# Kernel optimization log

Hardware: AMD Instinct MI355X
Metric: run time of the kernel (lower is better)

Reference implementation:

```python
import jax, jax.numpy as jnp
import numpy as np

B, S, D = 16, 2048, 512

def setup_inputs() -> dict:
    key = jax.random.key(0)
    ks = jax.random.split(key, 8)
    # xavier_uniform bound for [1,S,S]: sqrt(6/(S+S))
    bnd_attn = float(np.sqrt(6.0 / (S + S)))
    bnd_lin = float(np.sqrt(6.0 / (D + D)))
    return {
        "query": jax.random.normal(ks[0], (B, S, D), dtype=jnp.float32),
        "key": jax.random.normal(ks[1], (B, S, D), dtype=jnp.float32),
        "value": jax.random.normal(ks[2], (B, S, D), dtype=jnp.float32),
        "attn_bias": jax.random.uniform(ks[3], (1, S, S), minval=-bnd_attn, maxval=bnd_attn, dtype=jnp.float32),
        "Wq": jax.random.uniform(ks[4], (D, D), minval=-bnd_lin, maxval=bnd_lin, dtype=jnp.float32),
        "bq": jnp.zeros((D,), dtype=jnp.float32),
        "Wk": jax.random.uniform(ks[5], (D, D), minval=-bnd_lin, maxval=bnd_lin, dtype=jnp.float32),
        "bk": jnp.zeros((D,), dtype=jnp.float32),
    }

def reference(query, key, value, attn_bias, Wq, bq, Wk, bk):
    # q = query_fc(query); k = key_fc(key)  (torch Linear: x @ W.T + b)
    q = jnp.einsum('bsd,ed->bse', query, Wq) + bq            # [B,S,D]
    k = jnp.einsum('bsd,ed->bse', key, Wk) + bk              # [B,S,D]
    scores = attn_bias + jnp.einsum('bqd,bkd->bqk', q, k)    # [B,S,S]
    attention = jax.nn.softmax(scores, axis=-1)              # [B,S,S]
    out = jnp.einsum('bqk,bkd->bqd', attention, value)       # [B,S,D] (raw value, per source)
    return (out, attention)
```

## Files before the change

kernel.cpp:

```cpp
#include <hip/hip_runtime.h>


#define Bsz 16
#define Ssz 2048
#define Dsz 512
#define BK 32

#define AS1 __attribute__((address_space(1)))
#define AS3 __attribute__((address_space(3)))

typedef short bhalf8 __attribute__((ext_vector_type(8)));
typedef float f32x4 __attribute__((ext_vector_type(4)));
typedef unsigned short u16;

__device__ __forceinline__ u16 bf16_rn(float x) {
  unsigned u = __builtin_bit_cast(unsigned, x);
  u += 0x7fffu + ((u >> 16) & 1u);
  return (u16)(u >> 16);
}
__device__ __forceinline__ float bf16_f(u16 h) {
  unsigned u = ((unsigned)h) << 16;
  return __builtin_bit_cast(float, u);
}
__device__ __forceinline__ void gload16(const void* g, void* l) {
  __builtin_amdgcn_global_load_lds((const AS1 void*)g, (AS3 void*)l, 16, 0, 0);
}
__device__ __forceinline__ unsigned pk_bf16(float x, float y) {
  return (unsigned)bf16_rn(x) | ((unsigned)bf16_rn(y) << 16);
}

__global__ __launch_bounds__(256) void prep_w(const float* __restrict__ Wq,
                                              const float* __restrict__ Wk,
                                              u16* __restrict__ WTh,
                                              u16* __restrict__ WTl) {
  const int n = blockIdx.x >> 1;
  const int k = ((blockIdx.x & 1) << 8) + threadIdx.x;
  float acc = 0.f;
  for (int e = 0; e < Dsz; ++e)
    acc = fmaf(Wq[e * Dsz + k], Wk[e * Dsz + n], acc);
  const u16 h = bf16_rn(acc);
  WTh[n * Dsz + k] = h;
  WTl[n * Dsz + k] = bf16_rn(acc - bf16_f(h));
}

__global__ __launch_bounds__(256) void split_pair(const float* __restrict__ x,
                                                  u16* __restrict__ xh,
                                                  u16* __restrict__ xl, int n4) {
  const int i = blockIdx.x * 256 + threadIdx.x;
  if (i >= n4) return;
  const float4 v = ((const float4*)x)[i];
  const float xs[4] = {v.x, v.y, v.z, v.w};
  ushort4 h, l;
  u16* hp = (u16*)&h; u16* lp = (u16*)&l;
#pragma unroll
  for (int q = 0; q < 4; ++q) {
    hp[q] = bf16_rn(xs[q]);
    lp[q] = bf16_rn(xs[q] - bf16_f(hp[q]));
  }
  ((ushort4*)xh)[i] = h;
  ((ushort4*)xl)[i] = l;
}

__global__ __launch_bounds__(256) void transpose_v(const float* __restrict__ v,
                                                   u16* __restrict__ vT) {
  __shared__ u16 tile[64][65];
  const int b = blockIdx.z;
  const int d0 = blockIdx.x * 64, k0 = blockIdx.y * 64;
  const int c = threadIdx.x & 63, r4 = threadIdx.x >> 6;
  const float* vb = v + (long long)b * Ssz * Dsz;
  u16* vTb = vT + (long long)b * Dsz * Ssz;
#pragma unroll
  for (int p = 0; p < 16; ++p) {
    const int r = p * 4 + r4;
    tile[r][c] = bf16_rn(vb[(long long)(k0 + r) * Dsz + d0 + c]);
  }
  __syncthreads();
#pragma unroll
  for (int p = 0; p < 16; ++p) {
    const int cc = p * 4 + r4;
    vTb[(long long)(d0 + cc) * Ssz + k0 + c] = tile[c][cc];
  }
}

__global__ __launch_bounds__(256) void zero_f(float* __restrict__ p, int n) {
  const int i = blockIdx.x * 256 + threadIdx.x;
  if (i < n) p[i] = 0.f;
}

template <bool SPLIT_OUT>
__global__ __launch_bounds__(256) void gemm_split(
    const u16* __restrict__ Ahg, const u16* __restrict__ Alg, int lda, long long sA,
    const u16* __restrict__ Bhg, const u16* __restrict__ Blg, int ldb, long long sB,
    float* __restrict__ C, u16* __restrict__ Ch, u16* __restrict__ Cl, int ldc,
    long long sC, const float* __restrict__ bias, int K) {
  __shared__ u16 Ah[128 * 32], Al[128 * 32], Bh[128 * 32], Bl[128 * 32];
  const int tid = threadIdx.x, ln = tid & 63, wv = tid >> 6;
  const int wm = wv >> 1, wn = wv & 1;
  const int col = ln & 15, quad = ln >> 4;
  const int m0 = blockIdx.y * 128, n0 = blockIdx.x * 128;
  const long long z = blockIdx.z;
  const u16* Ahb = Ahg + z * sA; const u16* Alb = Alg + z * sA;
  const u16* Bhb = Bhg + z * sB; const u16* Blb = Blg + z * sB;

  long long aoff[2], boff[2];
  int lbase[2];
#pragma unroll
  for (int p = 0; p < 2; ++p) {
    const int cid = p * 256 + tid;
    const int row = cid >> 2;
    const int cg = (cid & 3) ^ ((row >> 1) & 3);
    aoff[p] = (long long)(m0 + row) * lda + cg * 8;
    boff[p] = (long long)(n0 + row) * ldb + cg * 8;
    lbase[p] = (p * 256 + wv * 64) * 8;
  }
  const int fsw = quad ^ ((col >> 1) & 3);
  const int aro = (wm * 64 + col) * 32 + fsw * 8;
  const int bro = (wn * 64 + col) * 32 + fsw * 8;

  f32x4 acc[4][4] = {};

  for (int kc = 0; kc < K; kc += BK) {
    __syncthreads();
#pragma unroll
    for (int p = 0; p < 2; ++p) {
      gload16(Ahb + aoff[p] + kc, &Ah[lbase[p]]);
      gload16(Alb + aoff[p] + kc, &Al[lbase[p]]);
      gload16(Bhb + boff[p] + kc, &Bh[lbase[p]]);
      gload16(Blb + boff[p] + kc, &Bl[lbase[p]]);
    }
    __syncthreads();
    bhalf8 ah[4], al[4], bh[4], bl[4];
#pragma unroll
    for (int i = 0; i < 4; ++i) {
      ah[i] = *(const bhalf8*)&Ah[aro + i * 16 * 32];
      al[i] = *(const bhalf8*)&Al[aro + i * 16 * 32];
      bh[i] = *(const bhalf8*)&Bh[bro + i * 16 * 32];
      bl[i] = *(const bhalf8*)&Bl[bro + i * 16 * 32];
    }
#pragma unroll
    for (int i = 0; i < 4; ++i)
#pragma unroll
      for (int j = 0; j < 4; ++j) {
        acc[i][j] = __builtin_amdgcn_mfma_f32_16x16x32_bf16(ah[i], bh[j], acc[i][j], 0, 0, 0);
        acc[i][j] = __builtin_amdgcn_mfma_f32_16x16x32_bf16(ah[i], bl[j], acc[i][j], 0, 0, 0);
        acc[i][j] = __builtin_amdgcn_mfma_f32_16x16x32_bf16(al[i], bh[j], acc[i][j], 0, 0, 0);
      }
  }

#pragma unroll
  for (int i = 0; i < 4; ++i) {
    const int mb = m0 + wm * 64 + (i << 4) + (quad << 2);
#pragma unroll
    for (int j = 0; j < 4; ++j) {
      const int n = n0 + wn * 64 + (j << 4) + col;
#pragma unroll
      for (int r = 0; r < 4; ++r) {
        const int m = mb + r;
        const float v = acc[i][j][r];
        if (SPLIT_OUT) {
          const u16 h = bf16_rn(v);
          Ch[(long long)m * ldc + n] = h;
          Cl[(long long)m * ldc + n] = bf16_rn(v - bf16_f(h));
        } else {
          C[z * sC + (long long)m * ldc + n] =
              v + bias[(long long)m * Ssz + n];
        }
      }
    }
  }
}

__global__ __launch_bounds__(256) void gemm_scores(
    const u16* __restrict__ Ahg, const u16* __restrict__ Alg,
    const u16* __restrict__ Bhg, const u16* __restrict__ Blg,
    const float* __restrict__ bias, float* __restrict__ C,
    float* __restrict__ rowsum) {
  __shared__ u16 Ah[128 * 32], Al[128 * 32], Bh[128 * 32], Bl[128 * 32];
  const int tid = threadIdx.x, ln = tid & 63, wv = tid >> 6;
  const int wm = wv >> 1, wn = wv & 1;
  const int col = ln & 15, quad = ln >> 4;
  const int m0 = blockIdx.y * 128, n0 = blockIdx.x * 128;
  const long long z = blockIdx.z;
  const long long zo = z * (long long)Ssz * Dsz;
  const u16* Ahb = Ahg + zo; const u16* Alb = Alg + zo;
  const u16* Bhb = Bhg + zo; const u16* Blb = Blg + zo;

  long long aoff[2], boff[2];
  int lbase[2];
#pragma unroll
  for (int p = 0; p < 2; ++p) {
    const int cid = p * 256 + tid;
    const int row = cid >> 2;
    const int cg = (cid & 3) ^ ((row >> 1) & 3);
    aoff[p] = (long long)(m0 + row) * Dsz + cg * 8;
    boff[p] = (long long)(n0 + row) * Dsz + cg * 8;
    lbase[p] = (p * 256 + wv * 64) * 8;
  }
  const int fsw = quad ^ ((col >> 1) & 3);
  const int aro = (wm * 64 + col) * 32 + fsw * 8;
  const int bro = (wn * 64 + col) * 32 + fsw * 8;

  f32x4 acc[4][4] = {};

  for (int kc = 0; kc < Dsz; kc += BK) {
    __syncthreads();
#pragma unroll
    for (int p = 0; p < 2; ++p) {
      gload16(Ahb + aoff[p] + kc, &Ah[lbase[p]]);
      gload16(Alb + aoff[p] + kc, &Al[lbase[p]]);
      gload16(Bhb + boff[p] + kc, &Bh[lbase[p]]);
      gload16(Blb + boff[p] + kc, &Bl[lbase[p]]);
    }
    __syncthreads();
    bhalf8 ah[4], al[4], bh[4], bl[4];
#pragma unroll
    for (int i = 0; i < 4; ++i) {
      ah[i] = *(const bhalf8*)&Ah[aro + i * 16 * 32];
      al[i] = *(const bhalf8*)&Al[aro + i * 16 * 32];
      bh[i] = *(const bhalf8*)&Bh[bro + i * 16 * 32];
      bl[i] = *(const bhalf8*)&Bl[bro + i * 16 * 32];
    }
#pragma unroll
    for (int i = 0; i < 4; ++i)
#pragma unroll
      for (int j = 0; j < 4; ++j) {
        acc[i][j] = __builtin_amdgcn_mfma_f32_16x16x32_bf16(ah[i], bh[j], acc[i][j], 0, 0, 0);
        acc[i][j] = __builtin_amdgcn_mfma_f32_16x16x32_bf16(ah[i], bl[j], acc[i][j], 0, 0, 0);
        acc[i][j] = __builtin_amdgcn_mfma_f32_16x16x32_bf16(al[i], bh[j], acc[i][j], 0, 0, 0);
      }
  }

  float* Cb = C + z * (long long)Ssz * Ssz;
  float* rsb = rowsum + z * Ssz;
#pragma unroll
  for (int i = 0; i < 4; ++i) {
    const int mb = m0 + wm * 64 + (i << 4) + (quad << 2);
#pragma unroll
    for (int r = 0; r < 4; ++r) {
      const int m = mb + r;
      float rs = 0.f;
#pragma unroll
      for (int j = 0; j < 4; ++j) {
        const int n = n0 + wn * 64 + (j << 4) + col;
        const float s = acc[i][j][r] + bias[(long long)m * Ssz + n];
        const float e = __expf(fminf(s - 80.f, 80.f));
        Cb[(long long)m * Ssz + n] = e;
        rs += e;
      }
      rs += __shfl_xor(rs, 1);
      rs += __shfl_xor(rs, 2);
      rs += __shfl_xor(rs, 4);
      rs += __shfl_xor(rs, 8);
      if (col == 0) atomicAdd(&rsb[m], rs);
    }
  }
}

__global__ __launch_bounds__(1024, 4) void pv_fused(
    float* __restrict__ attn,
    const float* __restrict__ rowsum,
    const u16* __restrict__ vT,
    float* __restrict__ out) {
  __shared__ u16 Vlds[2 * 16384];
  __shared__ u16 Plds[128 * 40];

  const int tid = threadIdx.x, ln = tid & 63, wv = tid >> 6;
  const int col = ln & 15, quad = ln >> 4;
  const int bid = blockIdx.x;
  const int xcd = bid & 7, k8 = bid >> 3;
  const int z = 2 * xcd + (k8 >> 4);
  const int m0 = (k8 & 15) * 128;

  float* Sb = attn + (long long)z * Ssz * Ssz + (long long)m0 * Ssz;
  const u16* vTb = vT + (long long)z * Dsz * Ssz;

  const int er = tid >> 3, es = tid & 7;
  const float eil = 1.0f / rowsum[(long long)z * Ssz + m0 + er];
  float* Srow = Sb + (long long)er * Ssz;

  int voff[2], vlb[2];
#pragma unroll
  for (int p = 0; p < 2; ++p) {
    const int q = p * 1024 + tid;
    const int row = q >> 2;
    const int cg = (q & 3) ^ ((row >> 1) & 3);
    voff[p] = row * Ssz + cg * 8;
    vlb[p] = (p * 1024 + wv * 64) * 8;
  }
  const int wm = wv >> 2, wn = wv & 3;
  const int apo = (wm * 32 + col) * 40;
  const int fsw = quad ^ ((col >> 1) & 3);
  const int bro = (wn * 128 + col) * 32 + fsw * 8;

  f32x4 acc[2][8] = {};

#pragma unroll
  for (int p = 0; p < 2; ++p) gload16(vTb + voff[p], &Vlds[vlb[p]]);
  float4 curS = *(const float4*)(Srow + es * 4);

  for (int t = 0; t < 64; ++t) {
    const int kc = t * 32, vb = t & 1;
    __syncthreads();
    float4 nextS = curS;
    if (t < 63) {
#pragma unroll
      for (int p = 0; p < 2; ++p)
        gload16(vTb + voff[p] + kc + 32, &Vlds[(vb ^ 1) * 16384 + vlb[p]]);
      nextS = *(const float4*)(Srow + kc + 32 + es * 4);
    }
    float4 p4;
    p4.x = curS.x * eil;
    p4.y = curS.y * eil;
    p4.z = curS.z * eil;
    p4.w = curS.w * eil;
    *(float4*)(Srow + kc + es * 4) = p4;
    uint2 pk;
    pk.x = pk_bf16(p4.x, p4.y);
    pk.y = pk_bf16(p4.z, p4.w);
    *(uint2*)&Plds[er * 40 + es * 4] = pk;
    asm volatile("s_waitcnt lgkmcnt(0)" ::: "memory");
    __builtin_amdgcn_s_barrier();
    asm volatile("" ::: "memory");
    bhalf8 pa[2];
#pragma unroll
    for (int i = 0; i < 2; ++i)
      pa[i] = *(const bhalf8*)&Plds[apo + i * 16 * 40 + quad * 8];
    __builtin_amdgcn_s_setprio(1);
#pragma unroll
    for (int j = 0; j < 8; ++j) {
      const bhalf8 vbv = *(const bhalf8*)&Vlds[vb * 16384 + bro + j * 16 * 32];
      acc[0][j] = __builtin_amdgcn_mfma_f32_16x16x32_bf16(pa[0], vbv, acc[0][j], 0, 0, 0);
      acc[1][j] = __builtin_amdgcn_mfma_f32_16x16x32_bf16(pa[1], vbv, acc[1][j], 0, 0, 0);
    }
    __builtin_amdgcn_s_setprio(0);
    curS = nextS;
  }

  float* ob = out + (long long)z * Ssz * Dsz;
#pragma unroll
  for (int i = 0; i < 2; ++i) {
    const int mb = m0 + wm * 32 + (i << 4) + (quad << 2);
#pragma unroll
    for (int j = 0; j < 8; ++j) {
      const int d = wn * 128 + (j << 4) + col;
#pragma unroll
      for (int r = 0; r < 4; ++r)
        ob[(long long)(mb + r) * Dsz + d] = acc[i][j][r];
    }
  }
}

extern "C" void kernel_launch(void* const* d_in, const int* in_sizes, int n_in,
                              void* d_out, int out_size, void* d_ws, size_t ws_size,
                              hipStream_t stream) {
  const float* query = (const float*)d_in[0];
  const float* key   = (const float*)d_in[1];
  const float* value = (const float*)d_in[2];
  const float* bias  = (const float*)d_in[3];
  const float* Wq    = (const float*)d_in[4];
  const float* Wk    = (const float*)d_in[6];

  float* outR  = (float*)d_out;
  float* attnR = outR + (long long)Bsz * Ssz * Dsz;

  u16* th = (u16*)outR;
  u16* tl = th + (long long)Bsz * Ssz * Dsz;

  char* w = (char*)d_ws;
  u16* vT  = (u16*)w;                                   w += (size_t)Bsz * Dsz * Ssz * 2;
  u16* WTh = (u16*)w;                                   w += (size_t)Dsz * Dsz * 2;
  u16* WTl = (u16*)w;                                   w += (size_t)Dsz * Dsz * 2;
  u16* qkh = (u16*)w;                                   w += (size_t)Bsz * Ssz * Dsz * 2;
  u16* qkl = (u16*)w;

  float* rowsum = (float*)WTh;

  const int nQK = Bsz * Ssz * Dsz;

  prep_w<<<dim3(1024), 256, 0, stream>>>(Wq, Wk, WTh, WTl);
  transpose_v<<<dim3(Dsz / 64, Ssz / 64, Bsz), 256, 0, stream>>>(value, vT);
  split_pair<<<dim3(nQK / 4 / 256), 256, 0, stream>>>(query, qkh, qkl, nQK / 4);

  gemm_split<true><<<dim3(Dsz / 128, (Bsz * Ssz) / 128, 1), 256, 0, stream>>>(
      qkh, qkl, Dsz, 0, WTh, WTl, Dsz, 0,
      nullptr, th, tl, Dsz, 0, nullptr, Dsz);

  split_pair<<<dim3(nQK / 4 / 256), 256, 0, stream>>>(key, qkh, qkl, nQK / 4);

  zero_f<<<dim3((Bsz * Ssz + 255) / 256), 256, 0, stream>>>(rowsum, Bsz * Ssz);

  gemm_scores<<<dim3(Ssz / 128, Ssz / 128, Bsz), 256, 0, stream>>>(
      th, tl, qkh, qkl, bias, attnR, rowsum);

  pv_fused<<<dim3(256), dim3(1024), 0, stream>>>(attnR, rowsum, vT, outR);
}
```

Before: 1.048 ms.

## Store unnormalized scores as bf16 workspace and write normalized attention in PV

```diff
diff --git a/kernel.cpp b/kernel.cpp
--- a/kernel.cpp
+++ b/kernel.cpp
@@ -170,6 +170,198 @@
   }
 }
 
+__global__ __launch_bounds__(256) void gemm_scores_b16(
+    const u16* __restrict__ Ahg, const u16* __restrict__ Alg,
+    const u16* __restrict__ Bhg, const u16* __restrict__ Blg,
+    const float* __restrict__ bias, u16* __restrict__ e16,
+    float* __restrict__ rowsum) {
+  __shared__ u16 Ah[128 * 32], Al[128 * 32], Bh[128 * 32], Bl[128 * 32];
+  const int tid = threadIdx.x, ln = tid & 63, wv = tid >> 6;
+  const int wm = wv >> 1, wn = wv & 1;
+  const int col = ln & 15, quad = ln >> 4;
+  const int bid = blockIdx.x;
+  const int sb = bid >> 8, wi = bid & 255;
+  const long long z = wi & 15;
+  const int n0 = ((sb & 3) * 4 + ((wi >> 4) & 3)) * 128;
+  const int m0 = ((sb >> 2) * 4 + (wi >> 6)) * 128;
+
+  const long long zo = z * (long long)Ssz * Dsz;
+  const u16* Ahb = Ahg + zo; const u16* Alb = Alg + zo;
+  const u16* Bhb = Bhg + zo; const u16* Blb = Blg + zo;
+
+  long long aoff[2], boff[2];
+  int lbase[2];
+#pragma unroll
+  for (int p = 0; p < 2; ++p) {
+    const int cid = p * 256 + tid;
+    const int row = cid >> 2;
+    const int cg = (cid & 3) ^ ((row >> 1) & 3);
+    aoff[p] = (long long)(m0 + row) * Dsz + cg * 8;
+    boff[p] = (long long)(n0 + row) * Dsz + cg * 8;
+    lbase[p] = (p * 256 + wv * 64) * 8;
+  }
+  const int fsw = quad ^ ((col >> 1) & 3);
+  const int aro = (wm * 64 + col) * 32 + fsw * 8;
+  const int bro = (wn * 64 + col) * 32 + fsw * 8;
+
+  f32x4 acc[4][4] = {};
+
+  for (int kc = 0; kc < Dsz; kc += BK) {
+    __syncthreads();
+#pragma unroll
+    for (int p = 0; p < 2; ++p) {
+      gload16(Ahb + aoff[p] + kc, &Ah[lbase[p]]);
+      gload16(Alb + aoff[p] + kc, &Al[lbase[p]]);
+      gload16(Bhb + boff[p] + kc, &Bh[lbase[p]]);
+      gload16(Blb + boff[p] + kc, &Bl[lbase[p]]);
+    }
+    __syncthreads();
+    bhalf8 ah[4], al[4], bh[4], bl[4];
+#pragma unroll
+    for (int i = 0; i < 4; ++i) {
+      ah[i] = *(const bhalf8*)&Ah[aro + i * 16 * 32];
+      al[i] = *(const bhalf8*)&Al[aro + i * 16 * 32];
+      bh[i] = *(const bhalf8*)&Bh[bro + i * 16 * 32];
+      bl[i] = *(const bhalf8*)&Bl[bro + i * 16 * 32];
+    }
+#pragma unroll
+    for (int i = 0; i < 4; ++i)
+#pragma unroll
+      for (int j = 0; j < 4; ++j) {
+        acc[i][j] = __builtin_amdgcn_mfma_f32_16x16x32_bf16(ah[i], bh[j], acc[i][j], 0, 0, 0);
+        acc[i][j] = __builtin_amdgcn_mfma_f32_16x16x32_bf16(ah[i], bl[j], acc[i][j], 0, 0, 0);
+        acc[i][j] = __builtin_amdgcn_mfma_f32_16x16x32_bf16(al[i], bh[j], acc[i][j], 0, 0, 0);
+      }
+  }
+
+  u16* Eb = e16 + z * (long long)Ssz * Ssz;
+  float* rsb = rowsum + z * Ssz;
+#pragma unroll
+  for (int i = 0; i < 4; ++i) {
+    const int mb = m0 + wm * 64 + (i << 4) + (quad << 2);
+#pragma unroll
+    for (int r = 0; r < 4; ++r) {
+      const int m = mb + r;
+      float rs = 0.f;
+#pragma unroll
+      for (int j = 0; j < 4; ++j) {
+        const int n = n0 + wn * 64 + (j << 4) + col;
+        const float s = acc[i][j][r] + bias[(long long)m * Ssz + n];
+        const u16 h = bf16_rn(__expf(fminf(s - 80.f, 80.f)));
+        Eb[(long long)m * Ssz + n] = h;
+        rs += bf16_f(h);
+      }
+      rs += __shfl_xor(rs, 1);
+      rs += __shfl_xor(rs, 2);
+      rs += __shfl_xor(rs, 4);
+      rs += __shfl_xor(rs, 8);
+      if (col == 0) atomicAdd(&rsb[m], rs);
+    }
+  }
+}
+
+__global__ __launch_bounds__(1024, 4) void pv_fused_b16(
+    const u16* __restrict__ e16,
+    const float* __restrict__ rowsum,
+    const u16* __restrict__ vT,
+    float* __restrict__ attn,
+    float* __restrict__ out) {
+  __shared__ u16 Elds[2 * 4096];
+  __shared__ u16 Vlds[2 * 16384];
+
+  const int tid = threadIdx.x, ln = tid & 63, wv = tid >> 6;
+  const int col = ln & 15, quad = ln >> 4;
+  const int bid = blockIdx.x;
+  const int xcd = bid & 7, k8 = bid >> 3;
+  const int z = 2 * xcd + (k8 >> 4);
+  const int m0 = (k8 & 15) * 128;
+
+  const u16* Eb = e16 + (long long)z * Ssz * Ssz + (long long)m0 * Ssz;
+  const u16* vTb = vT + (long long)z * Dsz * Ssz;
+  float* Pb = attn + (long long)z * Ssz * Ssz + (long long)m0 * Ssz;
+
+  const int er = tid >> 3, es = tid & 7;
+  const float eil = 1.0f / rowsum[(long long)z * Ssz + m0 + er];
+  float* Prow = Pb + (long long)er * Ssz;
+  const int elr = er * 32 + (((es >> 1) ^ ((er >> 1) & 3)) << 3) + (es & 1) * 4;
+
+  const int eq = tid;
+  const int erow = eq >> 2;
+  const int ecg = (eq & 3) ^ ((erow >> 1) & 3);
+  const int eoff = erow * Ssz + ecg * 8;
+  const int elbase = wv * 512;
+
+  int voff[2], vlb[2];
+#pragma unroll
+  for (int p = 0; p < 2; ++p) {
+    const int q = p * 1024 + tid;
+    const int row = q >> 2;
+    const int cg = (q & 3) ^ ((row >> 1) & 3);
+    voff[p] = row * Ssz + cg * 8;
+    vlb[p] = (p * 1024 + wv * 64) * 8;
+  }
+  const int wm = wv >> 2, wn = wv & 3;
+  const int fsw = quad ^ ((col >> 1) & 3);
+  const int aro = (wm * 32 + col) * 32 + fsw * 8;
+  const int bro = (wn * 128 + col) * 32 + fsw * 8;
+
+  f32x4 acc[2][8] = {};
+
+  if (wv < 8) gload16(Eb + eoff, &Elds[elbase]);
+#pragma unroll
+  for (int p = 0; p < 2; ++p) gload16(vTb + voff[p], &Vlds[vlb[p]]);
+
+  for (int t = 0; t < 64; ++t) {
+    const int kc = t * 32, vb = t & 1;
+    __syncthreads();
+    if (t < 63) {
+      if (wv < 8) gload16(Eb + eoff + kc + 32, &Elds[(vb ^ 1) * 4096 + elbase]);
+#pragma unroll
+      for (int p = 0; p < 2; ++p)
+        gload16(vTb + voff[p] + kc + 32, &Vlds[(vb ^ 1) * 16384 + vlb[p]]);
+    }
+    const uint2 eu = *(const uint2*)&Elds[vb * 4096 + elr];
+    float4 p4;
+    p4.x = __builtin_bit_cast(float, eu.x << 16) * eil;
+    p4.y = __builtin_bit_cast(float, eu.x & 0xffff0000u) * eil;
+    p4.z = __builtin_bit_cast(float, eu.y << 16) * eil;
+    p4.w = __builtin_bit_cast(float, eu.y & 0xffff0000u) * eil;
+    *(float4*)(Prow + kc + es * 4) = p4;
+    bhalf8 ah[2];
+#pragma unroll
+    for (int i = 0; i < 2; ++i)
+      ah[i] = *(const bhalf8*)&Elds[vb * 4096 + aro + i * 16 * 32];
+    __builtin_amdgcn_s_setprio(1);
+#pragma unroll
+    for (int j = 0; j < 8; ++j) {
+      const bhalf8 vbv = *(const bhalf8*)&Vlds[vb * 16384 + bro + j * 16 * 32];
+      acc[0][j] = __builtin_amdgcn_mfma_f32_16x16x32_bf16(ah[0], vbv, acc[0][j], 0, 0, 0);
+      acc[1][j] = __builtin_amdgcn_mfma_f32_16x16x32_bf16(ah[1], vbv, acc[1][j], 0, 0, 0);
+    }
+    __builtin_amdgcn_s_setprio(0);
+  }
+
+  float il[2][4];
+#pragma unroll
+  for (int i = 0; i < 2; ++i)
+#pragma unroll
+    for (int r = 0; r < 4; ++r)
+      il[i][r] = 1.0f /
+          rowsum[(long long)z * Ssz + m0 + wm * 32 + (i << 4) + (quad << 2) + r];
+  float* ob = out + (long long)z * Ssz * Dsz;
+#pragma unroll
+  for (int i = 0; i < 2; ++i) {
+    const int mb = m0 + wm * 32 + (i << 4) + (quad << 2);
+#pragma unroll
+    for (int j = 0; j < 8; ++j) {
+      const int d = wn * 128 + (j << 4) + col;
+#pragma unroll
+      for (int r = 0; r < 4; ++r)
+        ob[(long long)(mb + r) * Dsz + d] = acc[i][j][r] * il[i][r];
+    }
+  }
+}
+
 __global__ __launch_bounds__(256) void gemm_scores(
     const u16* __restrict__ Ahg, const u16* __restrict__ Alg,
     const u16* __restrict__ Bhg, const u16* __restrict__ Blg,
@@ -257,10 +449,8 @@
 }
 
 __global__ __launch_bounds__(1024, 4) void pv_fused(
-    float* __restrict__ attn,
-    const float* __restrict__ rowsum,
-    const u16* __restrict__ vT,
-    float* __restrict__ out) {
+    float* __restrict__ attn, const float* __restrict__ rowsum,
+    const u16* __restrict__ vT, float* __restrict__ out) {
   __shared__ u16 Vlds[2 * 16384];
   __shared__ u16 Plds[128 * 40];
 
@@ -371,9 +561,15 @@
   u16* WTh = (u16*)w;                                   w += (size_t)Dsz * Dsz * 2;
   u16* WTl = (u16*)w;                                   w += (size_t)Dsz * Dsz * 2;
   u16* qkh = (u16*)w;                                   w += (size_t)Bsz * Ssz * Dsz * 2;
-  u16* qkl = (u16*)w;
+  u16* qkl = (u16*)w;                                   w += (size_t)Bsz * Ssz * Dsz * 2;
+  u16* e16 = (u16*)w;
 
   float* rowsum = (float*)WTh;
+
+  const size_t NEED_B16 =
+      (size_t)Bsz * Dsz * Ssz * 2 + (size_t)Dsz * Dsz * 4 +
+      (size_t)Bsz * Ssz * Dsz * 4 + (size_t)Bsz * Ssz * Ssz * 2;
+  const bool useb16 = ws_size >= NEED_B16;
 
   const int nQK = Bsz * Ssz * Dsz;
 
@@ -389,8 +585,14 @@
 
   zero_f<<<dim3((Bsz * Ssz + 255) / 256), 256, 0, stream>>>(rowsum, Bsz * Ssz);
 
-  gemm_scores<<<dim3(Ssz / 128, Ssz / 128, Bsz), 256, 0, stream>>>(
-      th, tl, qkh, qkl, bias, attnR, rowsum);
-
-  pv_fused<<<dim3(256), dim3(1024), 0, stream>>>(attnR, rowsum, vT, outR);
-}
+  if (useb16) {
+    gemm_scores_b16<<<dim3(4096), 256, 0, stream>>>(th, tl, qkh, qkl, bias,
+                                                    e16, rowsum);
+    pv_fused_b16<<<dim3(256), dim3(1024), 0, stream>>>(e16, rowsum, vT, attnR,
+                                                       outR);
+  } else {
+    gemm_scores<<<dim3(Ssz / 128, Ssz / 128, Bsz), 256, 0, stream>>>(
+        th, tl, qkh, qkl, bias, attnR, rowsum);
+    pv_fused<<<dim3(256), dim3(1024), 0, stream>>>(attnR, rowsum, vT, outR);
+  }
+}
```

After: 980.3 us. 6.5% less time.
